# Performance work log

Measured on AMD Instinct MI355X. Metric: run time of the kernel, lower is better.

## Reference

```python
import jax, jax.numpy as jnp
import numpy as np

N_QUBITS = 8
N_LAYERS = 2
LN_EPS = 1e-5


def _ry(theta):
    # RY(t) = [[cos t/2, -sin t/2],[sin t/2, cos t/2]]; works batched or scalar
    c = jnp.cos(theta * 0.5)
    s = jnp.sin(theta * 0.5)
    return jnp.stack([jnp.stack([c, -s], -1), jnp.stack([s, c], -1)], -2).astype(jnp.complex64)


def _rz(theta):
    # RZ(t) = diag(e^{-it/2}, e^{it/2})
    e = jnp.exp(-0.5j * theta.astype(jnp.complex64))
    z = jnp.zeros_like(e)
    return jnp.stack([jnp.stack([e, z], -1), jnp.stack([z, jnp.conj(e)], -1)], -2)


def _apply_1q(psi, U, wire):
    # psi: (B, 2,...,2) with wire 0 most significant (PennyLane convention)
    ax = wire + 1
    psi = jnp.moveaxis(psi, ax, 1)
    psi = jnp.einsum('bpq,bq...->bp...', U, psi)
    return jnp.moveaxis(psi, 1, ax)


def _apply_cnot(psi, c, t):
    ca, ta = c + 1, t + 1
    psi = jnp.moveaxis(psi, (ca, ta), (1, 2))  # (B, 2c, 2t, rest)
    psi = jnp.stack([psi[:, 0], psi[:, 1, ::-1]], axis=1)  # flip target where control=1
    return jnp.moveaxis(psi, (1, 2), (ca, ta))


def _quantum(feats, q_weights):
    # feats: (B, 8) angle-encoded features; q_weights: (2, 8, 3)
    B = feats.shape[0]
    f = feats.astype(jnp.float32)
    psi = jnp.zeros((B,) + (2,) * N_QUBITS, jnp.complex64)
    psi = psi.at[(slice(None),) + (0,) * N_QUBITS].set(1.0)
    for l in range(N_LAYERS):
        for i in range(N_QUBITS):
            # gate order on wire i: RY(f_i), RZ(w0), RY(w1), RZ(w2)
            C = _rz(q_weights[l, i, 2]) @ _ry(q_weights[l, i, 1]) @ _rz(q_weights[l, i, 0])
            U = jnp.einsum('pq,bqr->bpr', C, _ry(f[:, i]))  # (B,2,2)
            psi = _apply_1q(psi, U, i)
        for i in range(N_QUBITS):
            psi = _apply_cnot(psi, i, (i + 1) % N_QUBITS)
    probs = jnp.abs(psi) ** 2  # (B, 2,...,2)
    zs = []
    for i in range(N_QUBITS):
        p = jnp.moveaxis(probs, i + 1, 1).reshape(B, 2, -1).sum(-1)
        zs.append(p[:, 0] - p[:, 1])  # <Z_i> = P(0) - P(1)
    return jnp.stack(zs, -1)  # (B, 8)


def setup_inputs() -> dict:
    key = jax.random.key(0)
    ks = jax.random.split(key, 12)
    B, D, H = 16384, 768, 256
    s = lambda fan_in: 1.0 / np.sqrt(fan_in)
    return {
        'x': jax.random.normal(ks[0], (B, D), jnp.float32),
        'W1': jax.random.uniform(ks[1], (D, H), jnp.float32, -s(D), s(D)),
        'b1': jax.random.uniform(ks[2], (H,), jnp.float32, -s(D), s(D)),
        'W2': jax.random.uniform(ks[3], (H, N_QUBITS), jnp.float32, -s(H), s(H)),
        'b2': jax.random.uniform(ks[4], (N_QUBITS,), jnp.float32, -s(H), s(H)),
        'q_weights': jax.random.normal(ks[5], (N_LAYERS, N_QUBITS, 3), jnp.float32) * 0.01,
        'W3': jax.random.uniform(ks[6], (N_QUBITS, H), jnp.float32, -s(N_QUBITS), s(N_QUBITS)),
        'b3': jax.random.uniform(ks[7], (H,), jnp.float32, -s(N_QUBITS), s(N_QUBITS)),
        'W4': jax.random.uniform(ks[8], (H, D), jnp.float32, -s(H), s(H)),
        'b4': jax.random.uniform(ks[9], (D,), jnp.float32, -s(H), s(H)),
        'gamma': jnp.ones((D,), jnp.float32),
        'beta': jnp.zeros((D,), jnp.float32),
    }


def reference(x, W1, b1, W2, b2, q_weights, W3, b3, W4, b4, gamma, beta):
    # classical compress (dropout = identity in eval)
    h = jax.nn.gelu(x @ W1 + b1, approximate=False)
    feats = h @ W2 + b2  # (B, 8) angle encoding
    z = _quantum(feats, q_weights)  # (B, 8) Pauli-Z expectations
    e = jax.nn.gelu(z @ W3 + b3, approximate=False)
    expanded = e @ W4 + b4
    y = x + expanded
    mu = y.mean(-1, keepdims=True)
    var = y.var(-1, keepdims=True)
    return gamma * (y - mu) / jnp.sqrt(var + LN_EPS) + beta
```

## Files before the change

kernel.cpp:

```cpp
#include <hip/hip_runtime.h>
#include <hip/hip_bf16.h>
#include <math.h>


typedef __attribute__((ext_vector_type(8))) short bf16x8;
typedef __attribute__((ext_vector_type(4))) float f32x4;

__device__ __forceinline__ float gelu_f(float x) {
    return 0.5f * x * (1.0f + erff(x * 0.70710678118654752f));
}

__device__ __forceinline__ short f2b(float x) {
    __hip_bfloat16 h = __float2bfloat16(x);
    return reinterpret_cast<short&>(h);
}

__device__ __forceinline__ short4 f4_to_b4(float4 v) {
    return make_short4(f2b(v.x), f2b(v.y), f2b(v.z), f2b(v.w));
}

__global__ __launch_bounds__(256) void transpose_bf16_kernel(
    const float* __restrict__ in, short* __restrict__ out, int K, int N)
{
    __shared__ float tl[32][33];
    const int k0 = blockIdx.y * 32, n0 = blockIdx.x * 32;
    const int r = threadIdx.x >> 3, c4 = (threadIdx.x & 7) * 4;
    const float4 v = *(const float4*)(in + (size_t)(k0 + r) * N + n0 + c4);
    tl[r][c4] = v.x; tl[r][c4 + 1] = v.y; tl[r][c4 + 2] = v.z; tl[r][c4 + 3] = v.w;
    __syncthreads();
    short4 o = make_short4(f2b(tl[c4][r]), f2b(tl[c4 + 1][r]),
                           f2b(tl[c4 + 2][r]), f2b(tl[c4 + 3][r]));
    *(short4*)(out + (size_t)(n0 + r) * K + k0 + c4) = o;
}

__global__ __launch_bounds__(256) void setup_kernel(
    const float* __restrict__ qw, const float* __restrict__ W2,
    float* __restrict__ Cg, short* __restrict__ W2T)
{
    const int t = threadIdx.x;
    if (t < 16) {
        const float w0 = qw[t * 3 + 0];
        const float w1 = qw[t * 3 + 1];
        const float w2 = qw[t * 3 + 2];
        const float a0 = 0.5f * w0, a2 = 0.5f * w2;
        float s1, c1; sincosf(0.5f * w1, &s1, &c1);
        float sp, cp; sincosf(a0 + a2, &sp, &cp);
        float sm, cm; sincosf(a0 - a2, &sm, &cm);
        Cg[t * 8 + 0] =  c1 * cp;  Cg[t * 8 + 1] = -c1 * sp;
        Cg[t * 8 + 2] = -s1 * cm;  Cg[t * 8 + 3] = -s1 * sm;
        Cg[t * 8 + 4] =  s1 * cm;  Cg[t * 8 + 5] = -s1 * sm;
        Cg[t * 8 + 6] =  c1 * cp;  Cg[t * 8 + 7] =  c1 * sp;
    }
    for (int idx = t; idx < 16 * 256; idx += 256) {
        const int n = idx & 15, k = idx >> 4;
        W2T[(size_t)n * 256 + k] = (n < 8) ? f2b(W2[(size_t)k * 8 + n]) : (short)0;
    }
}

__global__ __launch_bounds__(512) void gemm1_feats_kernel(
    const float* __restrict__ x, const short* __restrict__ W1bt,
    const float* __restrict__ b1, const short* __restrict__ W2T,
    const float* __restrict__ b2, float* __restrict__ feats, int M)
{
    __shared__ short As[2][64][40];
    __shared__ short hb[64][264];

    const int tid = threadIdx.x;
    const int wid = tid >> 6, L = tid & 63;
    const int quad = L >> 4, r16 = L & 15;
    const int mw = wid & 1, nw = wid >> 1;
    const int m0 = blockIdx.x * 64;

    const int m_s = tid >> 3, k_s = (tid & 7) << 2;
    const float* xp = x + (size_t)(m0 + m_s) * 768 + k_s;

    const short* bp = W1bt + (size_t)(nw * 64 + r16) * 768 + quad * 8;

    f32x4 acc[2][4];
    #pragma unroll
    for (int i = 0; i < 2; ++i)
        #pragma unroll
        for (int j = 0; j < 4; ++j) acc[i][j] = (f32x4){0.f, 0.f, 0.f, 0.f};

    float4 v0 = *(const float4*)(xp);
    *(short4*)&As[0][m_s][k_s] = f4_to_b4(v0);
    float4 v1 = *(const float4*)(xp + 32);
    __syncthreads();

    for (int kt = 0; kt < 24; ++kt) {
        const int buf = kt & 1;
        float4 vn = v1;
        if (kt + 2 < 24) vn = *(const float4*)(xp + (kt + 2) * 32);

        const bf16x8 a0 = *(const bf16x8*)&As[buf][32 * mw + r16][quad * 8];
        const bf16x8 a1 = *(const bf16x8*)&As[buf][32 * mw + 16 + r16][quad * 8];
        #pragma unroll
        for (int nt = 0; nt < 4; ++nt) {
            const bf16x8 bfr = *(const bf16x8*)(bp + (size_t)nt * 16 * 768 + kt * 32);
            acc[0][nt] = __builtin_amdgcn_mfma_f32_16x16x32_bf16(a0, bfr, acc[0][nt], 0, 0, 0);
            acc[1][nt] = __builtin_amdgcn_mfma_f32_16x16x32_bf16(a1, bfr, acc[1][nt], 0, 0, 0);
        }
        if (kt + 1 < 24) {
            *(short4*)&As[buf ^ 1][m_s][k_s] = f4_to_b4(v1);
        }
        __syncthreads();
        v1 = vn;
    }

    #pragma unroll
    for (int mt = 0; mt < 2; ++mt) {
        #pragma unroll
        for (int nt = 0; nt < 4; ++nt) {
            const int n = nw * 64 + nt * 16 + r16;
            const float bv = b1[n];
            #pragma unroll
            for (int reg = 0; reg < 4; ++reg) {
                const int rrow = 32 * mw + 16 * mt + quad * 4 + reg;
                hb[rrow][n] = f2b(gelu_f(acc[mt][nt][reg] + bv));
            }
        }
    }
    __syncthreads();

    if (wid < 4) {
        const int mt = wid;
        f32x4 fa = (f32x4){0.f, 0.f, 0.f, 0.f};
        #pragma unroll
        for (int kt = 0; kt < 8; ++kt) {
            const bf16x8 ha = *(const bf16x8*)&hb[16 * mt + r16][kt * 32 + quad * 8];
            const bf16x8 wb = *(const bf16x8*)(W2T + (size_t)r16 * 256 + kt * 32 + quad * 8);
            fa = __builtin_amdgcn_mfma_f32_16x16x32_bf16(ha, wb, fa, 0, 0, 0);
        }
        if (r16 < 8) {
            const float bv = b2[r16];
            #pragma unroll
            for (int reg = 0; reg < 4; ++reg) {
                const int row = m0 + 16 * mt + quad * 4 + reg;
                feats[(size_t)row * 8 + r16] = fa[reg] + bv;
            }
        }
    }
}

__global__ __launch_bounds__(256) void quantum_kernel(
    const float* __restrict__ feats, const float* __restrict__ Cg,
    const float* __restrict__ W3, const float* __restrict__ b3,
    short* __restrict__ ebt)
{
    const int t = threadIdx.x;
    const int wid = t >> 6, L = t & 63;
    const int row = blockIdx.x * 4 + wid;

    const float fv = feats[(size_t)row * 8 + (L & 7)];
    float sv, cv;
    sincosf(0.5f * fv, &sv, &cv);
    float cf[8], sf[8];
    #pragma unroll
    for (int w = 0; w < 8; ++w) {
        cf[w] = __shfl(cv, w, 64);
        sf[w] = __shfl(sv, w, 64);
    }

    float re[4], im[4];
    #pragma unroll
    for (int r = 0; r < 4; ++r) { re[r] = 0.0f; im[r] = 0.0f; }
    re[0] = (L == 0) ? 1.0f : 0.0f;

    const int G = L ^ (L >> 1);
    const int mapB = G ^ 48;
    const bool par = __popc(L) & 1;

    #pragma unroll
    for (int l = 0; l < 2; ++l) {
        #pragma unroll
        for (int w = 0; w < 8; ++w) {
            const float* Cw = Cg + (l * 8 + w) * 8;
            const float c0 = Cw[0], c1 = Cw[1], c2 = Cw[2], c3 = Cw[3];
            const float c4 = Cw[4], c5 = Cw[5], c6 = Cw[6], c7 = Cw[7];
            const float U00r = cf[w]*c0 + sf[w]*c2, U00i = cf[w]*c1 + sf[w]*c3;
            const float U01r = cf[w]*c2 - sf[w]*c0, U01i = cf[w]*c3 - sf[w]*c1;
            const float U10r = cf[w]*c4 + sf[w]*c6, U10i = cf[w]*c5 + sf[w]*c7;
            const float U11r = cf[w]*c6 - sf[w]*c4, U11i = cf[w]*c7 - sf[w]*c5;

            if (w <= 5) {
                const int kb = 5 - w;
                const int xm = 1 << kb;
                const bool hi = (L >> kb) & 1;
                const float u0r = hi ? U11r : U00r;
                const float u0i = hi ? U11i : U00i;
                const float u1r = hi ? U10r : U01r;
                const float u1i = hi ? U10i : U01i;
                #pragma unroll
                for (int r = 0; r < 4; ++r) {
                    const float ore = __shfl_xor(re[r], xm, 64);
                    const float oim = __shfl_xor(im[r], xm, 64);
                    const float nre = u0r*re[r] - u0i*im[r] + u1r*ore - u1i*oim;
                    const float nim = u0r*im[r] + u0i*re[r] + u1r*oim + u1i*ore;
                    re[r] = nre; im[r] = nim;
                }
            } else if (w == 6) {
                float nre[4], nim[4];
                #pragma unroll
                for (int p = 0; p < 2; ++p) {
                    nre[p]   = U00r*re[p]-U00i*im[p] + U01r*re[p+2]-U01i*im[p+2];
                    nim[p]   = U00r*im[p]+U00i*re[p] + U01r*im[p+2]+U01i*re[p+2];
                    nre[p+2] = U10r*re[p]-U10i*im[p] + U11r*re[p+2]-U11i*im[p+2];
                    nim[p+2] = U10r*im[p]+U10i*re[p] + U11r*im[p+2]+U11i*re[p+2];
                }
                #pragma unroll
                for (int r = 0; r < 4; ++r) { re[r] = nre[r]; im[r] = nim[r]; }
            } else {
                float nre[4], nim[4];
                #pragma unroll
                for (int p = 0; p < 4; p += 2) {
                    nre[p]   = U00r*re[p]-U00i*im[p] + U01r*re[p+1]-U01i*im[p+1];
                    nim[p]   = U00r*im[p]+U00i*re[p] + U01r*im[p+1]+U01i*re[p+1];
                    nre[p+1] = U10r*re[p]-U10i*im[p] + U11r*re[p+1]-U11i*im[p+1];
                    nim[p+1] = U10r*im[p]+U10i*re[p] + U11r*im[p+1]+U11i*re[p+1];
                }
                #pragma unroll
                for (int r = 0; r < 4; ++r) { re[r] = nre[r]; im[r] = nim[r]; }
            }
        }

        {
            const float s0r = par ? re[2] : re[0], s0i = par ? im[2] : im[0];
            const float s1r = par ? re[3] : re[1], s1i = par ? im[3] : im[1];
            const float s2r = par ? re[1] : re[3], s2i = par ? im[1] : im[3];
            const float s3r = par ? re[0] : re[2], s3i = par ? im[0] : im[2];
            re[0] = __shfl(s0r, G, 64);    im[0] = __shfl(s0i, G, 64);
            re[1] = __shfl(s1r, mapB, 64); im[1] = __shfl(s1i, mapB, 64);
            re[2] = __shfl(s2r, G, 64);    im[2] = __shfl(s2i, G, 64);
            re[3] = __shfl(s3r, mapB, 64); im[3] = __shfl(s3i, mapB, 64);
        }
    }

    const float p0 = re[0]*re[0] + im[0]*im[0];
    const float p1 = re[1]*re[1] + im[1]*im[1];
    const float p2 = re[2]*re[2] + im[2]*im[2];
    const float p3 = re[3]*re[3] + im[3]*im[3];
    const float pt = p0 + p1 + p2 + p3;
    float v[8];
    #pragma unroll
    for (int w = 0; w < 6; ++w) v[w] = ((L >> (5 - w)) & 1) ? -pt : pt;
    v[6] = p0 + p1 - p2 - p3;
    v[7] = p0 - p1 + p2 - p3;
    #pragma unroll
    for (int j = 0; j < 4; ++j) {
        const float send = (L & 1) ? v[j] : v[j + 4];
        const float keep = (L & 1) ? v[j + 4] : v[j];
        v[j] = keep + __shfl_xor(send, 1, 64);
    }
    #pragma unroll
    for (int j = 0; j < 2; ++j) {
        const float send = (L & 2) ? v[j] : v[j + 2];
        const float keep = (L & 2) ? v[j + 2] : v[j];
        v[j] = keep + __shfl_xor(send, 2, 64);
    }
    {
        const float send = (L & 4) ? v[0] : v[1];
        const float keep = (L & 4) ? v[1] : v[0];
        v[0] = keep + __shfl_xor(send, 4, 64);
    }
    v[0] += __shfl_xor(v[0], 8, 64);
    v[0] += __shfl_xor(v[0], 16, 64);
    v[0] += __shfl_xor(v[0], 32, 64);
    float z[8];
    #pragma unroll
    for (int w = 0; w < 8; ++w) {
        const int src = ((w & 1) << 2) | (w & 2) | ((w >> 2) & 1);
        z[w] = __shfl(v[0], src, 64);
    }

    const float4 b3v = *(const float4*)(b3 + 4 * L);
    float acc[4] = {b3v.x, b3v.y, b3v.z, b3v.w};
    #pragma unroll
    for (int w = 0; w < 8; ++w) {
        const float4 w3v = *(const float4*)(W3 + (size_t)w * 256 + 4 * L);
        acc[0] += z[w] * w3v.x; acc[1] += z[w] * w3v.y;
        acc[2] += z[w] * w3v.z; acc[3] += z[w] * w3v.w;
    }
    *(short4*)(ebt + (size_t)row * 256 + 4 * L) =
        make_short4(f2b(gelu_f(acc[0])), f2b(gelu_f(acc[1])),
                    f2b(gelu_f(acc[2])), f2b(gelu_f(acc[3])));
}

__global__ __launch_bounds__(256) void gemm4_ln_kernel(
    const short* __restrict__ ebt, const short* __restrict__ W4bt,
    const float* __restrict__ b4, const float* __restrict__ x,
    const float* __restrict__ gamma, const float* __restrict__ beta,
    float* __restrict__ out, int M)
{
    __shared__ short Ae[16][264];
    __shared__ float red[4][16][2];
    __shared__ float stats[16][2];

    const int tid = threadIdx.x;
    const int wv = tid >> 6, L = tid & 63;
    const int quad = L >> 4, r16 = L & 15;
    const int m0 = blockIdx.x * 16;
    const int n0 = wv * 192;

    {
        const int m_s = tid >> 4, k16 = (tid & 15) * 16;
        const int4* ep = (const int4*)(ebt + (size_t)(m0 + m_s) * 256 + k16);
        const int4 e0 = ep[0], e1 = ep[1];
        *(int4*)&Ae[m_s][k16] = e0;
        *(int4*)&Ae[m_s][k16 + 8] = e1;
    }
    __syncthreads();

    const short* bp = W4bt + (size_t)(n0 + r16) * 256 + quad * 8;

    f32x4 acc[12];
    #pragma unroll
    for (int nt = 0; nt < 12; ++nt) acc[nt] = (f32x4){0.f, 0.f, 0.f, 0.f};

    for (int kt = 0; kt < 8; ++kt) {
        const bf16x8 af = *(const bf16x8*)&Ae[r16][kt * 32 + quad * 8];
        #pragma unroll
        for (int nt = 0; nt < 12; ++nt) {
            const bf16x8 bfr = *(const bf16x8*)(bp + (size_t)nt * 16 * 256 + kt * 32);
            acc[nt] = __builtin_amdgcn_mfma_f32_16x16x32_bf16(af, bfr, acc[nt], 0, 0, 0);
        }
    }

    float ps[4] = {0.f, 0.f, 0.f, 0.f}, pq[4] = {0.f, 0.f, 0.f, 0.f};
    #pragma unroll
    for (int nt = 0; nt < 12; ++nt) {
        const int n = n0 + nt * 16 + r16;
        const float bv = b4[n];
        #pragma unroll
        for (int reg = 0; reg < 4; ++reg) {
            const int row = m0 + quad * 4 + reg;
            const float y = acc[nt][reg] + bv + x[(size_t)row * 768 + n];
            acc[nt][reg] = y;
            ps[reg] += y;
            pq[reg] += y * y;
        }
    }
    #pragma unroll
    for (int off = 1; off < 16; off <<= 1) {
        #pragma unroll
        for (int reg = 0; reg < 4; ++reg) {
            ps[reg] += __shfl_xor(ps[reg], off, 64);
            pq[reg] += __shfl_xor(pq[reg], off, 64);
        }
    }
    if (r16 == 0) {
        #pragma unroll
        for (int reg = 0; reg < 4; ++reg) {
            red[wv][quad * 4 + reg][0] = ps[reg];
            red[wv][quad * 4 + reg][1] = pq[reg];
        }
    }
    __syncthreads();
    if (tid < 16) {
        const float S = red[0][tid][0] + red[1][tid][0] + red[2][tid][0] + red[3][tid][0];
        const float Q = red[0][tid][1] + red[1][tid][1] + red[2][tid][1] + red[3][tid][1];
        const float mu = S * (1.0f / 768.0f);
        const float var = Q * (1.0f / 768.0f) - mu * mu;
        stats[tid][0] = mu;
        stats[tid][1] = rsqrtf(var + 1e-5f);
    }
    __syncthreads();

    float mu_r[4], rs_r[4];
    #pragma unroll
    for (int reg = 0; reg < 4; ++reg) {
        mu_r[reg] = stats[quad * 4 + reg][0];
        rs_r[reg] = stats[quad * 4 + reg][1];
    }
    #pragma unroll
    for (int nt = 0; nt < 12; ++nt) {
        const int n = n0 + nt * 16 + r16;
        const float g = gamma[n], bt = beta[n];
        #pragma unroll
        for (int reg = 0; reg < 4; ++reg) {
            const int row = m0 + quad * 4 + reg;
            out[(size_t)row * 768 + n] = g * (acc[nt][reg] - mu_r[reg]) * rs_r[reg] + bt;
        }
    }
}

extern "C" void kernel_launch(void* const* d_in, const int* in_sizes, int n_in,
                              void* d_out, int out_size, void* d_ws, size_t ws_size,
                              hipStream_t stream) {
    (void)n_in; (void)out_size; (void)ws_size;
    const float* x     = (const float*)d_in[0];
    const float* W1    = (const float*)d_in[1];
    const float* b1    = (const float*)d_in[2];
    const float* W2    = (const float*)d_in[3];
    const float* b2    = (const float*)d_in[4];
    const float* qw    = (const float*)d_in[5];
    const float* W3    = (const float*)d_in[6];
    const float* b3    = (const float*)d_in[7];
    const float* W4    = (const float*)d_in[8];
    const float* b4    = (const float*)d_in[9];
    const float* gamma = (const float*)d_in[10];
    const float* beta  = (const float*)d_in[11];
    float* out = (float*)d_out;

    const int D = 768, H = 256;
    const int B = in_sizes[0] / D;

    short* W1bt  = (short*)d_ws;
    short* W4bt  = W1bt + (size_t)H * D;
    short* W2T   = W4bt + (size_t)D * H;
    float* Cg    = (float*)(W2T + 16 * 256);
    float* feats = Cg + 128;
    short* ebt   = (short*)(feats + (size_t)B * 8);

    transpose_bf16_kernel<<<dim3(H / 32, D / 32), 256, 0, stream>>>(W1, W1bt, D, H);
    transpose_bf16_kernel<<<dim3(D / 32, H / 32), 256, 0, stream>>>(W4, W4bt, H, D);
    setup_kernel<<<1, 256, 0, stream>>>(qw, W2, Cg, W2T);
    gemm1_feats_kernel<<<dim3(B / 64), 512, 0, stream>>>(x, W1bt, b1, W2T, b2, feats, B);
    quantum_kernel<<<dim3(B / 4), 256, 0, stream>>>(feats, Cg, W3, b3, ebt);
    gemm4_ln_kernel<<<dim3(B / 16), 256, 0, stream>>>(ebt, W4bt, b4, x, gamma, beta, out, B);
}
```

Baseline: 234.1 us.

## Shrink gemm1 tiles to 32 rows and stage LayerNorm epilogue through LDS

gemm1 now processes 32 rows per block with 256 threads instead of 64 rows with 512. This doubles the grid, so more blocks can run across the CUs. The gemm4 epilogue writes MFMA accumulators to a shared-memory row buffer. Each thread then handles a contiguous row segment with float4 loads of x, b4, gamma and beta and float4 stores to out. The residual x loads are issued before the GEMM to hide their latency. This replaces strided scalar global accesses and a two-barrier cross-wave reduction, at the cost of about 49KB of LDS per block, which may limit occupancy.

```diff
diff --git a/kernel.cpp b/kernel.cpp
--- a/kernel.cpp
+++ b/kernel.cpp
@@ -57,19 +57,19 @@
     }
 }
 
-__global__ __launch_bounds__(512) void gemm1_feats_kernel(
+__global__ __launch_bounds__(256) void gemm1_feats_kernel(
     const float* __restrict__ x, const short* __restrict__ W1bt,
     const float* __restrict__ b1, const short* __restrict__ W2T,
     const float* __restrict__ b2, float* __restrict__ feats, int M)
 {
-    __shared__ short As[2][64][40];
-    __shared__ short hb[64][264];
+    __shared__ short As[2][32][40];
+    __shared__ short hb[32][264];
 
     const int tid = threadIdx.x;
     const int wid = tid >> 6, L = tid & 63;
     const int quad = L >> 4, r16 = L & 15;
-    const int mw = wid & 1, nw = wid >> 1;
-    const int m0 = blockIdx.x * 64;
+    const int nw = wid;
+    const int m0 = blockIdx.x * 32;
 
     const int m_s = tid >> 3, k_s = (tid & 7) << 2;
     const float* xp = x + (size_t)(m0 + m_s) * 768 + k_s;
@@ -92,8 +92,8 @@
         float4 vn = v1;
         if (kt + 2 < 24) vn = *(const float4*)(xp + (kt + 2) * 32);
 
-        const bf16x8 a0 = *(const bf16x8*)&As[buf][32 * mw + r16][quad * 8];
-        const bf16x8 a1 = *(const bf16x8*)&As[buf][32 * mw + 16 + r16][quad * 8];
+        const bf16x8 a0 = *(const bf16x8*)&As[buf][r16][quad * 8];
+        const bf16x8 a1 = *(const bf16x8*)&As[buf][16 + r16][quad * 8];
         #pragma unroll
         for (int nt = 0; nt < 4; ++nt) {
             const bf16x8 bfr = *(const bf16x8*)(bp + (size_t)nt * 16 * 768 + kt * 32);
@@ -115,14 +115,14 @@
             const float bv = b1[n];
             #pragma unroll
             for (int reg = 0; reg < 4; ++reg) {
-                const int rrow = 32 * mw + 16 * mt + quad * 4 + reg;
+                const int rrow = 16 * mt + quad * 4 + reg;
                 hb[rrow][n] = f2b(gelu_f(acc[mt][nt][reg] + bv));
             }
         }
     }
     __syncthreads();
 
-    if (wid < 4) {
+    if (wid < 2) {
         const int mt = wid;
         f32x4 fa = (f32x4){0.f, 0.f, 0.f, 0.f};
         #pragma unroll
@@ -292,14 +292,19 @@
     float* __restrict__ out, int M)
 {
     __shared__ short Ae[16][264];
-    __shared__ float red[4][16][2];
-    __shared__ float stats[16][2];
+    __shared__ float yb[16][772];
 
     const int tid = threadIdx.x;
     const int wv = tid >> 6, L = tid & 63;
     const int quad = L >> 4, r16 = L & 15;
     const int m0 = blockIdx.x * 16;
     const int n0 = wv * 192;
+
+    const int prow = tid >> 4, pcb = (tid & 15) * 4;
+    const float* xrow = x + (size_t)(m0 + prow) * 768 + pcb;
+    float4 xr[12];
+    #pragma unroll
+    for (int c = 0; c < 12; ++c) xr[c] = *(const float4*)(xrow + 64 * c);
 
     {
         const int m_s = tid >> 4, k16 = (tid & 15) * 16;
@@ -325,61 +330,50 @@
         }
     }
 
-    float ps[4] = {0.f, 0.f, 0.f, 0.f}, pq[4] = {0.f, 0.f, 0.f, 0.f};
     #pragma unroll
     for (int nt = 0; nt < 12; ++nt) {
         const int n = n0 + nt * 16 + r16;
-        const float bv = b4[n];
         #pragma unroll
         for (int reg = 0; reg < 4; ++reg) {
-            const int row = m0 + quad * 4 + reg;
-            const float y = acc[nt][reg] + bv + x[(size_t)row * 768 + n];
-            acc[nt][reg] = y;
-            ps[reg] += y;
-            pq[reg] += y * y;
-        }
+            yb[quad * 4 + reg][n] = acc[nt][reg];
+        }
+    }
+    __syncthreads();
+
+    float4 yv[12];
+    float s = 0.f, q = 0.f;
+    #pragma unroll
+    for (int c = 0; c < 12; ++c) {
+        const float4 b4v = *(const float4*)(b4 + pcb + 64 * c);
+        float4 y = *(const float4*)&yb[prow][pcb + 64 * c];
+        y.x += xr[c].x + b4v.x;
+        y.y += xr[c].y + b4v.y;
+        y.z += xr[c].z + b4v.z;
+        y.w += xr[c].w + b4v.w;
+        yv[c] = y;
+        s += y.x + y.y + y.z + y.w;
+        q += y.x * y.x + y.y * y.y + y.z * y.z + y.w * y.w;
     }
     #pragma unroll
     for (int off = 1; off < 16; off <<= 1) {
-        #pragma unroll
-        for (int reg = 0; reg < 4; ++reg) {
-            ps[reg] += __shfl_xor(ps[reg], off, 64);
-            pq[reg] += __shfl_xor(pq[reg], off, 64);
-        }
-    }
-    if (r16 == 0) {
-        #pragma unroll
-        for (int reg = 0; reg < 4; ++reg) {
-            red[wv][quad * 4 + reg][0] = ps[reg];
-            red[wv][quad * 4 + reg][1] = pq[reg];
-        }
-    }
-    __syncthreads();
-    if (tid < 16) {
-        const float S = red[0][tid][0] + red[1][tid][0] + red[2][tid][0] + red[3][tid][0];
-        const float Q = red[0][tid][1] + red[1][tid][1] + red[2][tid][1] + red[3][tid][1];
-        const float mu = S * (1.0f / 768.0f);
-        const float var = Q * (1.0f / 768.0f) - mu * mu;
-        stats[tid][0] = mu;
-        stats[tid][1] = rsqrtf(var + 1e-5f);
-    }
-    __syncthreads();
-
-    float mu_r[4], rs_r[4];
-    #pragma unroll
-    for (int reg = 0; reg < 4; ++reg) {
-        mu_r[reg] = stats[quad * 4 + reg][0];
-        rs_r[reg] = stats[quad * 4 + reg][1];
-    }
-    #pragma unroll
-    for (int nt = 0; nt < 12; ++nt) {
-        const int n = n0 + nt * 16 + r16;
-        const float g = gamma[n], bt = beta[n];
-        #pragma unroll
-        for (int reg = 0; reg < 4; ++reg) {
-            const int row = m0 + quad * 4 + reg;
-            out[(size_t)row * 768 + n] = g * (acc[nt][reg] - mu_r[reg]) * rs_r[reg] + bt;
-        }
+        s += __shfl_xor(s, off, 64);
+        q += __shfl_xor(q, off, 64);
+    }
+    const float mu = s * (1.0f / 768.0f);
+    const float var = q * (1.0f / 768.0f) - mu * mu;
+    const float rstd = rsqrtf(var + 1e-5f);
+
+    float* orow = out + (size_t)(m0 + prow) * 768 + pcb;
+    #pragma unroll
+    for (int c = 0; c < 12; ++c) {
+        const float4 gv = *(const float4*)(gamma + pcb + 64 * c);
+        const float4 bv = *(const float4*)(beta + pcb + 64 * c);
+        float4 o;
+        o.x = gv.x * (yv[c].x - mu) * rstd + bv.x;
+        o.y = gv.y * (yv[c].y - mu) * rstd + bv.y;
+        o.z = gv.z * (yv[c].z - mu) * rstd + bv.z;
+        o.w = gv.w * (yv[c].w - mu) * rstd + bv.w;
+        *(float4*)(orow + 64 * c) = o;
     }
 }
 
@@ -414,7 +408,7 @@
     transpose_bf16_kernel<<<dim3(H / 32, D / 32), 256, 0, stream>>>(W1, W1bt, D, H);
     transpose_bf16_kernel<<<dim3(D / 32, H / 32), 256, 0, stream>>>(W4, W4bt, H, D);
     setup_kernel<<<1, 256, 0, stream>>>(qw, W2, Cg, W2T);
-    gemm1_feats_kernel<<<dim3(B / 64), 512, 0, stream>>>(x, W1bt, b1, W2T, b2, feats, B);
+    gemm1_feats_kernel<<<dim3(B / 32), 256, 0, stream>>>(x, W1bt, b1, W2T, b2, feats, B);
     quantum_kernel<<<dim3(B / 4), 256, 0, stream>>>(feats, Cg, W3, b3, ebt);
     gemm4_ln_kernel<<<dim3(B / 16), 256, 0, stream>>>(ebt, W4bt, b4, x, gamma, beta, out, B);
 }
```

Measured after the change: 237.1 us. Within noise of the previous version (+1.3%).
